# Performance work log

Measured on AMD Instinct MI355X. Metric: run time of the kernel, lower is better.

The kernel has to match this reference:

```python
import jax, jax.numpy as jnp
import numpy as np

B, N, D, H = 8, 1024, 1024, 16
DH = D // H
EPS = 1e-6


def setup_inputs() -> dict:
    key = jax.random.key(0)
    ks = jax.random.split(key, 12)
    s = 1.0 / np.sqrt(D)
    inp = {
        "x": jax.random.normal(ks[0], (B, N, D), jnp.float32),
        "y": jax.random.normal(ks[1], (B, N, D), jnp.float32),
        "Wq": jax.random.normal(ks[2], (D, D), jnp.float32) * s,
        "bq": jnp.zeros((D,), jnp.float32),
        "Wk": jax.random.normal(ks[3], (D, D), jnp.float32) * s,
        "bk": jnp.zeros((D,), jnp.float32),
        "Wv": jax.random.normal(ks[4], (D, D), jnp.float32) * s,
        "bv": jnp.zeros((D,), jnp.float32),
        "Wf": jax.random.normal(ks[5], (D, D), jnp.float32) * s,
        "bf": jnp.zeros((D,), jnp.float32),
        "g1": jnp.ones((D,), jnp.float32),
        "b1": jnp.zeros((D,), jnp.float32),
        "g2": jnp.ones((D,), jnp.float32),
        "b2": jnp.zeros((D,), jnp.float32),
    }
    return inp


def _layernorm(x, g, b):
    mu = jnp.mean(x, axis=-1, keepdims=True)
    var = jnp.mean(jnp.square(x - mu), axis=-1, keepdims=True)
    return (x - mu) * jax.lax.rsqrt(var + EPS) * g + b


def reference(x, y, Wq, bq, Wk, bk, Wv, bv, Wf, bf, g1, b1, g2, b2):
    q = x @ Wq + bq                      # [B, Nq, D]
    k = y @ Wk + bk                      # [B, Nk, D]
    v = y @ Wv + bv                      # [B, Nk, D]
    qh = q.reshape(B, N, H, DH)
    kh = k.reshape(B, N, H, DH)
    vh = v.reshape(B, N, H, DH)
    # NOTE: original scales by sqrt(embed_dim), not sqrt(head_dim)
    scores = jnp.einsum("bqhd,bkhd->bhqk", qh, kh) / jnp.sqrt(jnp.float32(D))
    att = jax.nn.softmax(scores, axis=-1)
    o = jnp.einsum("bhqk,bkhd->bqhd", att, vh).reshape(B, N, D)
    out = x + o
    out = _layernorm(out, g1, b1)
    out = out + jax.nn.relu(out @ Wf + bf)
    out = _layernorm(out, g2, b2)
    return out
```

## Files before the change

### kernel.cpp

```cpp
#include <hip/hip_runtime.h>


#define Bb 8
#define Nn 1024
#define Dd 1024
#define Hh 16
#define DH 64
#define Mrows (Bb * 1024)

#define QSCL 0.045084220027780106f

typedef float f32x4 __attribute__((ext_vector_type(4)));
typedef __bf16 bf16x8 __attribute__((ext_vector_type(8)));
typedef unsigned int u32x4 __attribute__((ext_vector_type(4)));

#define MFMA16(acc, a, b) \
  acc = __builtin_amdgcn_mfma_f32_16x16x32_bf16((a), (b), (acc), 0, 0, 0)

__device__ __forceinline__ bf16x8 ld_frag(const void* p) {
  u32x4 v = *(const u32x4*)p;
  return __builtin_bit_cast(bf16x8, v);
}

__device__ __forceinline__ void gload16(const void* g, void* l) {
  __builtin_amdgcn_global_load_lds(
      (const __attribute__((address_space(1))) unsigned int*)g,
      (__attribute__((address_space(3))) unsigned int*)l, 16, 0, 0);
}

__device__ __forceinline__ unsigned short f2bf(float f) {
  return __builtin_bit_cast(unsigned short, (__bf16)f);
}
__device__ __forceinline__ float bf2f(unsigned short s) {
  unsigned int u = ((unsigned int)s) << 16;
  return __builtin_bit_cast(float, u);
}
__device__ __forceinline__ unsigned cvt_pk_bf16(float a, float b) {
  unsigned r;
  asm("v_cvt_pk_bf16_f32 %0, %1, %2" : "=v"(r) : "v"(a), "v"(b));
  return r;
}

__global__ __launch_bounds__(256) void cvt_f32_bf16_2(
    const float* __restrict__ in0, unsigned short* __restrict__ out0,
    const float* __restrict__ in1, unsigned short* __restrict__ out1, int n4) {
  const float* in = blockIdx.y ? in1 : in0;
  unsigned short* out = blockIdx.y ? out1 : out0;
  int i = blockIdx.x * blockDim.x + threadIdx.x;
  int stride = gridDim.x * blockDim.x;
  for (; i < n4; i += stride) {
    float4 v = ((const float4*)in)[i];
    ushort4 o;
    o.x = f2bf(v.x); o.y = f2bf(v.y); o.z = f2bf(v.z); o.w = f2bf(v.w);
    ((ushort4*)out)[i] = o;
  }
}

__global__ __launch_bounds__(256) void transpose_cvt4(
    const float* __restrict__ W0, const float* __restrict__ W1,
    const float* __restrict__ W2, const float* __restrict__ W3,
    unsigned short* __restrict__ T0, unsigned short* __restrict__ T1,
    unsigned short* __restrict__ T2, unsigned short* __restrict__ T3) {
  __shared__ float tile[32][33];
  const float* W = blockIdx.z == 0 ? W0 : blockIdx.z == 1 ? W1
                   : blockIdx.z == 2 ? W2 : W3;
  unsigned short* Wt = blockIdx.z == 0 ? T0 : blockIdx.z == 1 ? T1
                       : blockIdx.z == 2 ? T2 : T3;
  int tx = threadIdx.x, ty = threadIdx.y;
  int n0 = blockIdx.x * 32, k0 = blockIdx.y * 32;
#pragma unroll
  for (int i = ty; i < 32; i += 8)
    tile[i][tx] = W[(size_t)(k0 + i) * Dd + n0 + tx];
  __syncthreads();
#pragma unroll
  for (int i = ty; i < 32; i += 8)
    Wt[(size_t)(n0 + i) * Dd + k0 + tx] = f2bf(tile[tx][i]);
}

struct GemmCtx { int m0, n0, wm, wn, lr, lk, lg, l, w; };

template <typename EpiFn>
__device__ __forceinline__ void gemm_core(
    const unsigned short* __restrict__ A, const unsigned short* __restrict__ Bt,
    int K, EpiFn epi) {
  __shared__ __attribute__((aligned(16))) unsigned short As[2][128 * 32];
  __shared__ __attribute__((aligned(16))) unsigned short Bs[2][128 * 32];
  const int bid = blockIdx.y * 8 + blockIdx.x;
  const int nwg = (gridDim.x * gridDim.y);
  const int swz = (bid & 7) * (nwg >> 3) + (bid >> 3);
  const int m0 = (swz >> 3) * 128, n0 = (swz & 7) * 128;
  const int t = threadIdx.x, w = t >> 6, l = t & 63;
  const int wm = (w >> 1) * 64, wn = (w & 1) * 64;
  const int lr = l & 15, lk = (l >> 4) * 8;
  const int rA = t >> 2, sA = (t & 3) * 8;
  char* AsB = (char*)As;
  char* BsB = (char*)Bs;
  const int wb = (w * 64) * 16;

  f32x4 acc[4][4] = {};

  for (int k0 = 0; k0 < K; k0 += 64) {
    __syncthreads();
#pragma unroll
    for (int h = 0; h < 2; ++h) {
      const int ko = k0 + h * 32;
      gload16(A + (size_t)(m0 + rA) * K + ko + sA, AsB + h * 8192 + wb);
      gload16(A + (size_t)(m0 + 64 + rA) * K + ko + sA, AsB + h * 8192 + wb + 4096);
      gload16(Bt + (size_t)(n0 + rA) * K + ko + sA, BsB + h * 8192 + wb);
      gload16(Bt + (size_t)(n0 + 64 + rA) * K + ko + sA, BsB + h * 8192 + wb + 4096);
    }
    __syncthreads();

#pragma unroll
    for (int h = 0; h < 2; ++h) {
      bf16x8 af[4], bfr[4];
#pragma unroll
      for (int i = 0; i < 4; ++i)
        af[i] = ld_frag(&As[h][(wm + i * 16 + lr) * 32 + lk]);
#pragma unroll
      for (int j = 0; j < 4; ++j)
        bfr[j] = ld_frag(&Bs[h][(wn + j * 16 + lr) * 32 + lk]);
#pragma unroll
      for (int i = 0; i < 4; ++i)
#pragma unroll
        for (int j = 0; j < 4; ++j) MFMA16(acc[i][j], af[i], bfr[j]);
    }
  }
  GemmCtx c{m0, n0, wm, wn, lr, lk, l >> 4, l, w};
  epi(acc, c);
}

__global__ __launch_bounds__(256) void gemm_qkv(
    const unsigned short* __restrict__ xb, const unsigned short* __restrict__ yb,
    const unsigned short* __restrict__ WqT, const unsigned short* __restrict__ WkT,
    const unsigned short* __restrict__ WvT,
    const float* __restrict__ bq, const float* __restrict__ bk,
    const float* __restrict__ bv,
    unsigned short* __restrict__ Qb, unsigned short* __restrict__ Kb,
    unsigned short* __restrict__ Vtb) {
  const int z = blockIdx.z;
  const unsigned short* A = (z == 0) ? xb : yb;
  const unsigned short* Bt = (z == 0) ? WqT : (z == 1) ? WkT : WvT;
  const float* bias = (z == 0) ? bq : (z == 1) ? bk : bv;
  unsigned short* Cb = (z == 0) ? Qb : Kb;

  gemm_core(A, Bt, Dd, [&](f32x4 (&acc)[4][4], GemmCtx c) {
#pragma unroll
    for (int i = 0; i < 4; ++i)
#pragma unroll
      for (int j = 0; j < 4; ++j) {
        int col = c.n0 + c.wn + j * 16 + c.lr;
        float bcol = bias[col];
        if (z == 2) {
          int brow = c.m0 + c.wm + i * 16 + c.lg * 4;
          int bi = brow >> 10, nloc = brow & 1023;
          ushort4 o4;
          o4.x = f2bf(acc[i][j][0] + bcol);
          o4.y = f2bf(acc[i][j][1] + bcol);
          o4.z = f2bf(acc[i][j][2] + bcol);
          o4.w = f2bf(acc[i][j][3] + bcol);
          *(ushort4*)(Vtb + ((size_t)bi * Dd + col) * Nn + nloc) = o4;
        } else {
          float scl = (z == 0) ? QSCL : 1.0f;
#pragma unroll
          for (int r = 0; r < 4; ++r) {
            int row = c.m0 + c.wm + i * 16 + c.lg * 4 + r;
            Cb[(size_t)row * Dd + col] = f2bf((acc[i][j][r] + bcol) * scl);
          }
        }
      }
  });
}

__global__ __launch_bounds__(256) void gemm_ff(
    const unsigned short* __restrict__ A, const unsigned short* __restrict__ Bt,
    const float* __restrict__ bias, const unsigned short* __restrict__ Tres,
    unsigned short* __restrict__ Cb) {
  gemm_core(A, Bt, Dd, [&](f32x4 (&acc)[4][4], GemmCtx c) {
#pragma unroll
    for (int i = 0; i < 4; ++i)
#pragma unroll
      for (int j = 0; j < 4; ++j) {
        int col = c.n0 + c.wn + j * 16 + c.lr;
        float bcol = bias[col];
#pragma unroll
        for (int r = 0; r < 4; ++r) {
          int row = c.m0 + c.wm + i * 16 + c.lg * 4 + r;
          size_t idx = (size_t)row * Dd + col;
          Cb[idx] = f2bf(bf2f(Tres[idx]) + fmaxf(acc[i][j][r] + bcol, 0.f));
        }
      }
  });
}

__global__ __launch_bounds__(256) void attn_fwd(
    const unsigned short* __restrict__ Qg, const unsigned short* __restrict__ Kg,
    const unsigned short* __restrict__ Vt, unsigned short* __restrict__ Obf) {
  __shared__ __attribute__((aligned(16))) unsigned short Ks[64 * 64];
  __shared__ __attribute__((aligned(16))) unsigned short Vts[64 * 64];
  char* KsB = (char*)Ks;
  char* VtsB = (char*)Vts;

  const int bid = blockIdx.y * 8 + blockIdx.x;
  const int swz = (bid & 7) * 128 + (bid >> 3);
  const int q0 = (swz & 7) * 128;
  const int by = swz >> 3;
  const int b = by >> 4, h = by & 15;

  const int t = threadIdx.x, w = t >> 6, l = t & 63;
  const int lr = l & 15, lg = l >> 4;

  bf16x8 aq[2][2];
#pragma unroll
  for (int i = 0; i < 2; ++i) {
    const unsigned short* qp =
        Qg + ((size_t)b * Nn + q0 + w * 32 + i * 16 + lr) * Dd + h * DH + lg * 8;
    aq[i][0] = *(const bf16x8*)qp;
    aq[i][1] = *(const bf16x8*)(qp + 32);
  }

  const size_t baseK = (size_t)b * Nn * Dd + h * DH;
  const size_t baseV = ((size_t)b * Dd + h * DH) * Nn;

  const int srow = t >> 3, sch = t & 7;
  const int sby = srow * 128 + ((sch * 16) ^ ((srow & 7) << 4));
  const int sby2 = sby + 32 * 128;

  uint4 kA = *(const uint4*)(Kg + baseK + (size_t)srow * Dd + sch * 8);
  uint4 kB = *(const uint4*)(Kg + baseK + (size_t)(srow + 32) * Dd + sch * 8);
  uint4 vA = *(const uint4*)(Vt + baseV + (size_t)srow * Nn + sch * 8);
  uint4 vB = *(const uint4*)(Vt + baseV + (size_t)(srow + 32) * Nn + sch * 8);

  f32x4 oacc[4][2] = {};
  float lp[2] = {0.f, 0.f};

  const int fx = (lg * 16) ^ ((lr & 7) << 4);

  for (int kv = 0; kv < Nn / 64; ++kv) {
    __syncthreads();
    *(uint4*)(KsB + sby) = kA;
    *(uint4*)(KsB + sby2) = kB;
    *(uint4*)(VtsB + sby) = vA;
    *(uint4*)(VtsB + sby2) = vB;
    __syncthreads();

    if (kv + 1 < Nn / 64) {
      int kvo = (kv + 1) * 64;
      kA = *(const uint4*)(Kg + baseK + (size_t)(kvo + srow) * Dd + sch * 8);
      kB = *(const uint4*)(Kg + baseK + (size_t)(kvo + srow + 32) * Dd + sch * 8);
      vA = *(const uint4*)(Vt + baseV + (size_t)srow * Nn + kvo + sch * 8);
      vB = *(const uint4*)(Vt + baseV + (size_t)(srow + 32) * Nn + kvo + sch * 8);
    }

    f32x4 st[2][4];
    __builtin_amdgcn_s_setprio(1);
#pragma unroll
    for (int j = 0; j < 4; ++j) {
      const int kro = (j * 16 + lr) * 128;
      bf16x8 k0 = ld_frag(KsB + kro + fx);
      bf16x8 k1 = ld_frag(KsB + kro + (fx ^ 64));
#pragma unroll
      for (int i = 0; i < 2; ++i) {
        f32x4 z = {0.f, 0.f, 0.f, 0.f};
        MFMA16(z, k0, aq[i][0]);
        MFMA16(z, k1, aq[i][1]);
        st[i][j] = z;
      }
    }
    __builtin_amdgcn_s_setprio(0);

#pragma unroll
    for (int i = 0; i < 2; ++i) {
      float s = 0.f;
#pragma unroll
      for (int j = 0; j < 4; ++j) {
        float e0 = exp2f(st[i][j][0]);
        float e1 = exp2f(st[i][j][1]);
        float e2 = exp2f(st[i][j][2]);
        float e3 = exp2f(st[i][j][3]);
        st[i][j][0] = e0; st[i][j][1] = e1; st[i][j][2] = e2; st[i][j][3] = e3;
        s += (e0 + e1) + (e2 + e3);
      }
      lp[i] += s;
    }

#pragma unroll
    for (int m = 0; m < 2; ++m) {
      bf16x8 pb[2];
#pragma unroll
      for (int i = 0; i < 2; ++i) {
        u32x4 pk;
        pk[0] = cvt_pk_bf16(st[i][2 * m][0], st[i][2 * m][1]);
        pk[1] = cvt_pk_bf16(st[i][2 * m][2], st[i][2 * m][3]);
        pk[2] = cvt_pk_bf16(st[i][2 * m + 1][0], st[i][2 * m + 1][1]);
        pk[3] = cvt_pk_bf16(st[i][2 * m + 1][2], st[i][2 * m + 1][3]);
        pb[i] = __builtin_bit_cast(bf16x8, pk);
      }
      __builtin_amdgcn_s_setprio(1);
#pragma unroll
      for (int da = 0; da < 4; ++da) {
        const int vrow = da * 16 + lr;
        const int vbase = vrow * 128;
        const int vswz = (vrow & 7) << 4;
        uint2 a0 = *(const uint2*)(VtsB + vbase + ((64 * m + 8 * lg) ^ vswz));
        uint2 a1 = *(const uint2*)(VtsB + vbase + ((64 * m + 32 + 8 * lg) ^ vswz));
        u32x4 av = {a0.x, a0.y, a1.x, a1.y};
        bf16x8 va = __builtin_bit_cast(bf16x8, av);
        MFMA16(oacc[da][0], va, pb[0]);
        MFMA16(oacc[da][1], va, pb[1]);
      }
      __builtin_amdgcn_s_setprio(0);
    }
  }

#pragma unroll
  for (int i = 0; i < 2; ++i) {
    float s = lp[i];
    s += __shfl_xor(s, 16, 64);
    s += __shfl_xor(s, 32, 64);
    float rd = 1.f / s;
    const size_t orow = (size_t)b * Nn + q0 + w * 32 + i * 16 + lr;
#pragma unroll
    for (int da = 0; da < 4; ++da) {
      ushort4 o4;
      o4.x = f2bf(oacc[da][i][0] * rd);
      o4.y = f2bf(oacc[da][i][1] * rd);
      o4.z = f2bf(oacc[da][i][2] * rd);
      o4.w = f2bf(oacc[da][i][3] * rd);
      *(ushort4*)(Obf + orow * Dd + h * DH + da * 16 + lg * 4) = o4;
    }
  }
}

template <int MODE>
__global__ __launch_bounds__(256) void ln_k(
    const unsigned short* __restrict__ X, const unsigned short* __restrict__ Oin,
    const float* __restrict__ gamma, const float* __restrict__ beta,
    unsigned short* __restrict__ out_bf, float* __restrict__ out_f) {
  __shared__ float red[8];
  const int row = blockIdx.x, t = threadIdx.x;
  ushort4 xu = ((const ushort4*)(X + (size_t)row * Dd))[t];
  float4 v = {bf2f(xu.x), bf2f(xu.y), bf2f(xu.z), bf2f(xu.w)};
  if (MODE == 0) {
    ushort4 o = ((const ushort4*)(Oin + (size_t)row * Dd))[t];
    v.x += bf2f(o.x); v.y += bf2f(o.y); v.z += bf2f(o.z); v.w += bf2f(o.w);
  }
  float s = v.x + v.y + v.z + v.w;
#pragma unroll
  for (int o = 32; o > 0; o >>= 1) s += __shfl_xor(s, o, 64);
  if ((t & 63) == 0) red[t >> 6] = s;
  __syncthreads();
  float mean = (red[0] + red[1] + red[2] + red[3]) * (1.f / 1024.f);
  float dx = v.x - mean, dy = v.y - mean, dz = v.z - mean, dw = v.w - mean;
  float s2 = dx * dx + dy * dy + dz * dz + dw * dw;
#pragma unroll
  for (int o = 32; o > 0; o >>= 1) s2 += __shfl_xor(s2, o, 64);
  if ((t & 63) == 0) red[4 + (t >> 6)] = s2;
  __syncthreads();
  float var = (red[4] + red[5] + red[6] + red[7]) * (1.f / 1024.f);
  float rstd = rsqrtf(var + 1e-6f);
  float4 g = ((const float4*)gamma)[t];
  float4 bb = ((const float4*)beta)[t];
  float r0 = dx * rstd * g.x + bb.x;
  float r1 = dy * rstd * g.y + bb.y;
  float r2 = dz * rstd * g.z + bb.z;
  float r3 = dw * rstd * g.w + bb.w;
  if (MODE == 0) {
    ushort4 o4;
    o4.x = f2bf(r0); o4.y = f2bf(r1); o4.z = f2bf(r2); o4.w = f2bf(r3);
    ((ushort4*)(out_bf + (size_t)row * Dd))[t] = o4;
  } else {
    float4 o4 = {r0, r1, r2, r3};
    ((float4*)(out_f + (size_t)row * Dd))[t] = o4;
  }
}

extern "C" void kernel_launch(void* const* d_in, const int* in_sizes, int n_in,
                              void* d_out, int out_size, void* d_ws, size_t ws_size,
                              hipStream_t stream) {
  const float* x  = (const float*)d_in[0];
  const float* y  = (const float*)d_in[1];
  const float* Wq = (const float*)d_in[2];
  const float* bq = (const float*)d_in[3];
  const float* Wk = (const float*)d_in[4];
  const float* bk = (const float*)d_in[5];
  const float* Wv = (const float*)d_in[6];
  const float* bv = (const float*)d_in[7];
  const float* Wf = (const float*)d_in[8];
  const float* bf = (const float*)d_in[9];
  const float* g1 = (const float*)d_in[10];
  const float* b1 = (const float*)d_in[11];
  const float* g2 = (const float*)d_in[12];
  const float* b2 = (const float*)d_in[13];

  char* ws = (char*)d_ws;
  const size_t MB = 1024 * 1024;
  unsigned short* xb  = (unsigned short*)(ws + 0 * MB);
  unsigned short* yb  = (unsigned short*)(ws + 16 * MB);
  unsigned short* WqT = (unsigned short*)(ws + 32 * MB);
  unsigned short* WkT = (unsigned short*)(ws + 34 * MB);
  unsigned short* WvT = (unsigned short*)(ws + 36 * MB);
  unsigned short* WfT = (unsigned short*)(ws + 38 * MB);
  unsigned short* Qb  = (unsigned short*)(ws + 40 * MB);
  unsigned short* Kb  = (unsigned short*)(ws + 56 * MB);
  unsigned short* Vtb = (unsigned short*)(ws + 72 * MB);
  unsigned short* Obf = (unsigned short*)(ws + 16 * MB);
  unsigned short* tb  = (unsigned short*)(ws + 40 * MB);
  unsigned short* ub  = (unsigned short*)(ws + 56 * MB);

  const int n4 = (Mrows * Dd) / 4;
  cvt_f32_bf16_2<<<dim3(1024, 2), 256, 0, stream>>>(x, xb, y, yb, n4);

  transpose_cvt4<<<dim3(32, 32, 4), dim3(32, 8), 0, stream>>>(
      Wq, Wk, Wv, Wf, WqT, WkT, WvT, WfT);

  gemm_qkv<<<dim3(8, 64, 3), 256, 0, stream>>>(
      xb, yb, WqT, WkT, WvT, bq, bk, bv, Qb, Kb, Vtb);

  attn_fwd<<<dim3(8, 128), 256, 0, stream>>>(Qb, Kb, Vtb, Obf);

  ln_k<0><<<Mrows, 256, 0, stream>>>(xb, Obf, g1, b1, tb, nullptr);

  gemm_ff<<<dim3(8, 64), 256, 0, stream>>>(tb, WfT, bf, tb, ub);

  ln_k<1><<<Mrows, 256, 0, stream>>>(ub, nullptr, g2, b2, nullptr, (float*)d_out);
}
```

Before: 216.2 us.

## Permute V^T storage for single 16-byte LDS loads and compute softmax sums via MFMA

The V projection epilogue now writes V^T with a permuted sequence index, so the attention kernel can fetch each V fragment with one 16-byte LDS load instead of two 8-byte loads. The softmax row sums are now taken from an MFMA of the bf16-rounded probabilities against a ones vector, replacing the per-lane float accumulation and cross-lane shuffles. This cuts LDS instructions and VALU adds in the inner loop, at the cost of two extra MFMAs per sub-block. The sums now use the same bf16-rounded probabilities as the numerator, which slightly changes numerics.

New measurement: 208.3 us. 3.6% less time.

```diff
diff --git a/kernel.cpp b/kernel.cpp
--- a/kernel.cpp
+++ b/kernel.cpp
@@ -154,12 +154,14 @@
         if (z == 2) {
           int brow = c.m0 + c.wm + i * 16 + c.lg * 4;
           int bi = brow >> 10, nloc = brow & 1023;
+          int nperm = (nloc & ~31) | (((nloc >> 2) & 3) << 3) |
+                      (((nloc >> 4) & 1) << 2);
           ushort4 o4;
           o4.x = f2bf(acc[i][j][0] + bcol);
           o4.y = f2bf(acc[i][j][1] + bcol);
           o4.z = f2bf(acc[i][j][2] + bcol);
           o4.w = f2bf(acc[i][j][3] + bcol);
-          *(ushort4*)(Vtb + ((size_t)bi * Dd + col) * Nn + nloc) = o4;
+          *(ushort4*)(Vtb + ((size_t)bi * Dd + col) * Nn + nperm) = o4;
         } else {
           float scl = (z == 0) ? QSCL : 1.0f;
 #pragma unroll
@@ -219,6 +221,9 @@
     aq[i][1] = *(const bf16x8*)(qp + 32);
   }
 
+  u32x4 one4 = {0x3F803F80u, 0x3F803F80u, 0x3F803F80u, 0x3F803F80u};
+  const bf16x8 vones = __builtin_bit_cast(bf16x8, one4);
+
   const size_t baseK = (size_t)b * Nn * Dd + h * DH;
   const size_t baseV = ((size_t)b * Dd + h * DH) * Nn;
 
@@ -232,9 +237,7 @@
   uint4 vB = *(const uint4*)(Vt + baseV + (size_t)(srow + 32) * Nn + sch * 8);
 
   f32x4 oacc[4][2] = {};
-  float lp[2] = {0.f, 0.f};
-
-  const int fx = (lg * 16) ^ ((lr & 7) << 4);
+  f32x4 lacc[2] = {};
 
   for (int kv = 0; kv < Nn / 64; ++kv) {
     __syncthreads();
@@ -257,8 +260,9 @@
 #pragma unroll
     for (int j = 0; j < 4; ++j) {
       const int kro = (j * 16 + lr) * 128;
-      bf16x8 k0 = ld_frag(KsB + kro + fx);
-      bf16x8 k1 = ld_frag(KsB + kro + (fx ^ 64));
+      const int ksw = ((lg ^ ((lr & 7))) << 4);
+      bf16x8 k0 = ld_frag(KsB + kro + (((lg ^ (lr & 7))) << 4));
+      bf16x8 k1 = ld_frag(KsB + kro + ((((lg + 4) ^ (lr & 7))) << 4));
 #pragma unroll
       for (int i = 0; i < 2; ++i) {
         f32x4 z = {0.f, 0.f, 0.f, 0.f};
@@ -270,19 +274,14 @@
     __builtin_amdgcn_s_setprio(0);
 
 #pragma unroll
-    for (int i = 0; i < 2; ++i) {
-      float s = 0.f;
+    for (int i = 0; i < 2; ++i)
 #pragma unroll
       for (int j = 0; j < 4; ++j) {
-        float e0 = exp2f(st[i][j][0]);
-        float e1 = exp2f(st[i][j][1]);
-        float e2 = exp2f(st[i][j][2]);
-        float e3 = exp2f(st[i][j][3]);
-        st[i][j][0] = e0; st[i][j][1] = e1; st[i][j][2] = e2; st[i][j][3] = e3;
-        s += (e0 + e1) + (e2 + e3);
-      }
-      lp[i] += s;
-    }
+        st[i][j][0] = exp2f(st[i][j][0]);
+        st[i][j][1] = exp2f(st[i][j][1]);
+        st[i][j][2] = exp2f(st[i][j][2]);
+        st[i][j][3] = exp2f(st[i][j][3]);
+      }
 
 #pragma unroll
     for (int m = 0; m < 2; ++m) {
@@ -297,15 +296,13 @@
         pb[i] = __builtin_bit_cast(bf16x8, pk);
       }
       __builtin_amdgcn_s_setprio(1);
+      MFMA16(lacc[0], vones, pb[0]);
+      MFMA16(lacc[1], vones, pb[1]);
 #pragma unroll
       for (int da = 0; da < 4; ++da) {
         const int vrow = da * 16 + lr;
-        const int vbase = vrow * 128;
-        const int vswz = (vrow & 7) << 4;
-        uint2 a0 = *(const uint2*)(VtsB + vbase + ((64 * m + 8 * lg) ^ vswz));
-        uint2 a1 = *(const uint2*)(VtsB + vbase + ((64 * m + 32 + 8 * lg) ^ vswz));
-        u32x4 av = {a0.x, a0.y, a1.x, a1.y};
-        bf16x8 va = __builtin_bit_cast(bf16x8, av);
+        bf16x8 va = ld_frag(
+            VtsB + vrow * 128 + (((lg + 4 * m) ^ (vrow & 7)) << 4));
         MFMA16(oacc[da][0], va, pb[0]);
         MFMA16(oacc[da][1], va, pb[1]);
       }
@@ -315,10 +312,7 @@
 
 #pragma unroll
   for (int i = 0; i < 2; ++i) {
-    float s = lp[i];
-    s += __shfl_xor(s, 16, 64);
-    s += __shfl_xor(s, 32, 64);
-    float rd = 1.f / s;
+    float rd = 1.f / lacc[i][0];
     const size_t orow = (size_t)b * Nn + q0 + w * 32 + i * 16 + lr;
 #pragma unroll
     for (int da = 0; da < 4; ++da) {
```
